# Kernel tuning notes

Hardware: AMD Instinct MI355X
Metric: run time of the kernel (lower is better)

Reference implementation:

```python
import jax, jax.numpy as jnp
import numpy as np

NUM_BINS = 23
SIGMA_RATIO = 0.5
SMOOTH_NR = 1e-07
SMOOTH_DR = 1e-07

BIN_CENTERS = jnp.linspace(0.0, 1.0, NUM_BINS)  # [bins]
_sigma = jnp.mean(BIN_CENTERS[1:] - BIN_CENTERS[:-1]) * SIGMA_RATIO
PRETERM = 1.0 / (2.0 * _sigma ** 2)


def setup_inputs() -> dict:
    key = jax.random.key(0)
    k1, k2 = jax.random.split(key)
    shape = (4, 1, 96, 96, 96)
    pred = jax.random.uniform(k1, shape, dtype=jnp.float32)
    target = jax.random.uniform(k2, shape, dtype=jnp.float32)
    return {"pred": pred, "target": target}


def _parzen(img):
    # img: [B, ...] -> weight [B, N, bins], probability [B, 1, bins]
    img = jnp.clip(img, 0.0, 1.0)
    img = img.reshape(img.shape[0], -1, 1)  # [B, N, 1]
    weight = jnp.exp(-PRETERM * (img - BIN_CENTERS[None, None, :]) ** 2)  # [B, N, bins]
    weight = weight / jnp.sum(weight, axis=-1, keepdims=True)
    probability = jnp.mean(weight, axis=-2, keepdims=True)  # [B, 1, bins]
    return weight, probability


def reference(pred, target):
    wa, pa = _parzen(pred)    # wa: [B, N, bins]
    wb, pb = _parzen(target)
    n = wa.shape[1]
    # joint histogram: [B, bins, bins]
    pab = jnp.einsum('bni,bnj->bij', wa, wb) / n
    # marginal product: [B, bins, bins]
    papb = jnp.einsum('bki,bkj->bij', pa, pb)
    mi = jnp.sum(pab * jnp.log((pab + SMOOTH_NR) / (papb + SMOOTH_DR) + SMOOTH_DR), axis=(1, 2))
    return -jnp.mean(mi)
```

## Files before the change

### kernel.cpp

```cpp
#include <hip/hip_runtime.h>
#include <math.h>


#define NBINS   23
#define NCELLS  529
#define NBATCH  4
#define NVOX    884736
#define PBLK    432
#define RPB     16
#define RBLK    (PBLK / RPB)
#define RS      72
#define IMGB    (32 * RS * 2)
#define WREG    (2 * IMGB)

typedef float    vf4  __attribute__((ext_vector_type(4)));
typedef _Float16 h8   __attribute__((ext_vector_type(8)));
typedef float    f16v __attribute__((ext_vector_type(16)));

#define G1 0.13533528f
#define G2 3.3546263e-4f
#define G3 1.5229979e-8f

__device__ __forceinline__ float window7(float x, int& i0, float* w)
{
    x = fminf(fmaxf(x, 0.0f), 1.0f);
    int ka = (int)floorf(fmaf(x, 22.0f, 0.5f));
    i0 = min(max(ka - 3, 0), 16);
    float v  = fmaf((float)(i0 + 3), -(1.0f / 22.0f), x);
    float W0 = __expf(-968.0f * v * v);
    float R  = __expf(88.0f * v);
    float Ri = __builtin_amdgcn_rcpf(R);
    float R2 = R * R,   R3 = R2 * R;
    float R2i = Ri * Ri, R3i = R2i * Ri;
    w[0] = W0 * (R3i * G3);
    w[1] = W0 * (R2i * G2);
    w[2] = W0 * (Ri  * G1);
    w[3] = W0;
    w[4] = W0 * (R   * G1);
    w[5] = W0 * (R2  * G2);
    w[6] = W0 * (R3  * G3);
    return ((w[0] + w[6]) + (w[1] + w[5])) + ((w[2] + w[4]) + w[3]);
}

__global__ __launch_bounds__(256)
void mi_mfma(const float* __restrict__ pred,
             const float* __restrict__ targ,
             float* __restrict__ partial)
{
    __shared__ __align__(16) char smem[4 * WREG];

    const int p    = blockIdx.x;
    const int b    = blockIdx.y;
    const int wv   = threadIdx.x >> 6;
    const int lane = threadIdx.x & 63;
    const int m    = lane & 31;
    const int h    = lane >> 5;

    char* wbase = smem + wv * WREG;
    _Float16* Aimg = (_Float16*)wbase;
    _Float16* Bimg = (_Float16*)(wbase + IMGB);

    const size_t base = (size_t)b * NVOX + (size_t)p * 2048 + (size_t)wv * 512
                      + (size_t)lane * 8;
    const vf4* __restrict__ px4 = (const vf4*)(pred + base);
    const vf4* __restrict__ py4 = (const vf4*)(targ + base);
    vf4 xa = px4[0], xb = px4[1], ya = py4[0], yb = py4[1];
    float xs[8] = {xa.x, xa.y, xa.z, xa.w, xb.x, xb.y, xb.z, xb.w};
    float ys[8] = {ya.x, ya.y, ya.z, ya.w, yb.x, yb.y, yb.z, yb.w};

    f16v acc = {};

    #pragma unroll
    for (int c = 0; c < 8; ++c) {
        vf4 z = {0.f, 0.f, 0.f, 0.f};
        #pragma unroll
        for (int it = 0; it < 3; ++it) {
            *(vf4*)(wbase        + (it * 64 + lane) * 16) = z;
            *(vf4*)(wbase + IMGB + (it * 64 + lane) * 16) = z;
        }
        if (lane < 24) {
            *(vf4*)(wbase        + (192 + lane) * 16) = z;
            *(vf4*)(wbase + IMGB + (192 + lane) * 16) = z;
        }

        int ia, ja;
        float wa[7], wb[7];
        float sa = window7(xs[c], ia, wa);
        float sb = window7(ys[c], ja, wb);
        float inv = __builtin_amdgcn_rcpf(sa * sb);

        #pragma unroll
        for (int t = 0; t < 7; ++t) {
            Aimg[(ia + t) * RS + lane] = (_Float16)(wa[t] * inv);
            Bimg[(ja + t) * RS + lane] = (_Float16)wb[t];
        }

        #pragma unroll
        for (int s = 0; s < 4; ++s) {
            h8 Af = *(const h8*)(Aimg + m * RS + 16 * s + 8 * h);
            h8 Bf = *(const h8*)(Bimg + m * RS + 16 * s + 8 * h);
            acc = __builtin_amdgcn_mfma_f32_32x32x16_f16(Af, Bf, acc, 0, 0, 0);
        }
    }

    float* tile = (float*)wbase;
    #pragma unroll
    for (int r = 0; r < 16; ++r) {
        int row = (r & 3) + 8 * (r >> 2) + 4 * h;
        tile[row * 33 + m] = acc[r];
    }
    __syncthreads();
    for (int c = threadIdx.x; c < NCELLS; c += 256) {
        int i = c / NBINS, j = c % NBINS;
        float s = 0.0f;
        #pragma unroll
        for (int w = 0; w < 4; ++w)
            s += ((const float*)(smem + w * WREG))[i * 33 + j];
        partial[((size_t)(b * PBLK + p)) * NCELLS + c] = s;
    }
}

__global__ __launch_bounds__(256)
void mi_reduce(const float* __restrict__ partial, double* __restrict__ pab64)
{
    const int g = blockIdx.x;
    const int b = blockIdx.y;
    const int t = threadIdx.x;
    const float* __restrict__ src =
        partial + ((size_t)b * PBLK + (size_t)g * RPB) * NCELLS;

    double a0 = 0.0, a1 = 0.0, a2 = 0.0;
    #pragma unroll
    for (int p = 0; p < RPB; ++p) {
        const float* __restrict__ row = src + (size_t)p * NCELLS;
        a0 += (double)row[t];
        a1 += (double)row[256 + t];
        if (t < NCELLS - 512) a2 += (double)row[512 + t];
    }
    atomicAdd(&pab64[b * NCELLS + t],       a0);
    atomicAdd(&pab64[b * NCELLS + 256 + t], a1);
    if (t < NCELLS - 512) atomicAdd(&pab64[b * NCELLS + 512 + t], a2);
}

__global__ __launch_bounds__(256)
void mi_final(const double* __restrict__ pab64, float* __restrict__ out)
{
    __shared__ double s_pab[NCELLS];
    __shared__ double s_pa[NBINS];
    __shared__ double s_pb[NBINS];
    __shared__ double s_red[4];

    double total = 0.0;
    for (int b = 0; b < NBATCH; ++b) {
        for (int c = threadIdx.x; c < NCELLS; c += 256)
            s_pab[c] = pab64[b * NCELLS + c] * (1.0 / (double)NVOX);
        __syncthreads();
        if (threadIdx.x < NBINS) {
            const int i = threadIdx.x;
            double r = 0.0, cl = 0.0;
            for (int j = 0; j < NBINS; ++j) {
                r  += s_pab[i * NBINS + j];
                cl += s_pab[j * NBINS + i];
            }
            s_pa[i] = r; s_pb[i] = cl;
        }
        __syncthreads();
        double t = 0.0;
        for (int c = threadIdx.x; c < NCELLS; c += 256) {
            double pv   = s_pab[c];
            double papb = s_pa[c / NBINS] * s_pb[c % NBINS];
            t += pv * log((pv + 1e-7) / (papb + 1e-7) + 1e-7);
        }
        #pragma unroll
        for (int off = 32; off > 0; off >>= 1) t += __shfl_down(t, off, 64);
        if ((threadIdx.x & 63) == 0) s_red[threadIdx.x >> 6] = t;
        __syncthreads();
        if (threadIdx.x == 0) total += s_red[0] + s_red[1] + s_red[2] + s_red[3];
        __syncthreads();
    }
    if (threadIdx.x == 0) out[0] = (float)(-total * 0.25);
}

extern "C" void kernel_launch(void* const* d_in, const int* in_sizes, int n_in,
                              void* d_out, int out_size, void* d_ws, size_t ws_size,
                              hipStream_t stream)
{
    const float* pred = (const float*)d_in[0];
    const float* targ = (const float*)d_in[1];
    float* out = (float*)d_out;
    char* ws = (char*)d_ws;

    const size_t off_partial = 0;
    const size_t off_pab64   =
        ((size_t)NBATCH * PBLK * NCELLS * 4 + 255) & ~(size_t)255;

    float*  partial = (float*)(ws + off_partial);
    double* pab64   = (double*)(ws + off_pab64);

    (void)hipMemsetAsync(pab64, 0, (size_t)NBATCH * NCELLS * sizeof(double), stream);
    mi_mfma  <<<dim3(PBLK, NBATCH), 256, 0, stream>>>(pred, targ, partial);
    mi_reduce<<<dim3(RBLK, NBATCH), 256, 0, stream>>>(partial, pab64);
    mi_final <<<1, 256, 0, stream>>>(pab64, out);
}
```

Baseline: 107.8 us.

## Fold memset and final kernel into neighbors, swizzle LDS weight images

Removes the hipMemsetAsync and the separate single-block final kernel. The first block of each batch in the MFMA kernel now zeroes the accumulators and the flag. The reduce kernel uses a last-block-done atomic counter to run the MI computation. It also XOR-swizzles the fp16 weight image columns in LDS to cut bank conflicts on the writes and MFMA operand reads. This trades launch overhead for threadfence and atomic-counter synchronization.

```diff
diff --git a/kernel.cpp b/kernel.cpp
--- a/kernel.cpp
+++ b/kernel.cpp
@@ -12,6 +12,8 @@
 #define RS      72
 #define IMGB    (32 * RS * 2)
 #define WREG    (2 * IMGB)
+
+#define SWZ(r, c) ((c) ^ (((r) & 7) << 3))
 
 typedef float    vf4  __attribute__((ext_vector_type(4)));
 typedef _Float16 h8   __attribute__((ext_vector_type(8)));
@@ -45,7 +47,9 @@
 __global__ __launch_bounds__(256)
 void mi_mfma(const float* __restrict__ pred,
              const float* __restrict__ targ,
-             float* __restrict__ partial)
+             float* __restrict__ partial,
+             double* __restrict__ pab64,
+             unsigned int* __restrict__ flag)
 {
     __shared__ __align__(16) char smem[4 * WREG];
 
@@ -55,6 +59,12 @@
     const int lane = threadIdx.x & 63;
     const int m    = lane & 31;
     const int h    = lane >> 5;
+
+    if (p == 0) {
+        for (int c = threadIdx.x; c < NCELLS; c += 256)
+            pab64[b * NCELLS + c] = 0.0;
+        if (b == 0 && threadIdx.x == 0) *flag = 0u;
+    }
 
     char* wbase = smem + wv * WREG;
     _Float16* Aimg = (_Float16*)wbase;
@@ -91,14 +101,15 @@
 
         #pragma unroll
         for (int t = 0; t < 7; ++t) {
-            Aimg[(ia + t) * RS + lane] = (_Float16)(wa[t] * inv);
-            Bimg[(ja + t) * RS + lane] = (_Float16)wb[t];
+            int ra = ia + t, rb = ja + t;
+            Aimg[ra * RS + SWZ(ra, lane)] = (_Float16)(wa[t] * inv);
+            Bimg[rb * RS + SWZ(rb, lane)] = (_Float16)wb[t];
         }
 
         #pragma unroll
         for (int s = 0; s < 4; ++s) {
-            h8 Af = *(const h8*)(Aimg + m * RS + 16 * s + 8 * h);
-            h8 Bf = *(const h8*)(Bimg + m * RS + 16 * s + 8 * h);
+            h8 Af = *(const h8*)(Aimg + m * RS + SWZ(m, 16 * s + 8 * h));
+            h8 Bf = *(const h8*)(Bimg + m * RS + SWZ(m, 16 * s + 8 * h));
             acc = __builtin_amdgcn_mfma_f32_32x32x16_f16(Af, Bf, acc, 0, 0, 0);
         }
     }
@@ -121,7 +132,10 @@
 }
 
 __global__ __launch_bounds__(256)
-void mi_reduce(const float* __restrict__ partial, double* __restrict__ pab64)
+void mi_reduce_final(const float* __restrict__ partial,
+                     double* __restrict__ pab64,
+                     unsigned int* __restrict__ flag,
+                     float* __restrict__ out)
 {
     const int g = blockIdx.x;
     const int b = blockIdx.y;
@@ -140,45 +154,52 @@
     atomicAdd(&pab64[b * NCELLS + t],       a0);
     atomicAdd(&pab64[b * NCELLS + 256 + t], a1);
     if (t < NCELLS - 512) atomicAdd(&pab64[b * NCELLS + 512 + t], a2);
-}
-
-__global__ __launch_bounds__(256)
-void mi_final(const double* __restrict__ pab64, float* __restrict__ out)
-{
+
+    __threadfence();
+    __shared__ int is_last;
+    if (t == 0)
+        is_last = (atomicAdd(flag, 1u) == (unsigned)(RBLK * NBATCH - 1));
+    __syncthreads();
+    if (!is_last) return;
+    __threadfence();
+
     __shared__ double s_pab[NCELLS];
     __shared__ double s_pa[NBINS];
     __shared__ double s_pb[NBINS];
     __shared__ double s_red[4];
 
     double total = 0.0;
-    for (int b = 0; b < NBATCH; ++b) {
-        for (int c = threadIdx.x; c < NCELLS; c += 256)
-            s_pab[c] = pab64[b * NCELLS + c] * (1.0 / (double)NVOX);
-        __syncthreads();
-        if (threadIdx.x < NBINS) {
-            const int i = threadIdx.x;
+    for (int bb = 0; bb < NBATCH; ++bb) {
+        for (int c = t; c < NCELLS; c += 256) {
+            double v = __hip_atomic_load(&pab64[bb * NCELLS + c],
+                                         __ATOMIC_RELAXED,
+                                         __HIP_MEMORY_SCOPE_AGENT);
+            s_pab[c] = v * (1.0 / (double)NVOX);
+        }
+        __syncthreads();
+        if (t < NBINS) {
             double r = 0.0, cl = 0.0;
             for (int j = 0; j < NBINS; ++j) {
-                r  += s_pab[i * NBINS + j];
-                cl += s_pab[j * NBINS + i];
+                r  += s_pab[t * NBINS + j];
+                cl += s_pab[j * NBINS + t];
             }
-            s_pa[i] = r; s_pb[i] = cl;
-        }
-        __syncthreads();
-        double t = 0.0;
-        for (int c = threadIdx.x; c < NCELLS; c += 256) {
+            s_pa[t] = r; s_pb[t] = cl;
+        }
+        __syncthreads();
+        double s = 0.0;
+        for (int c = t; c < NCELLS; c += 256) {
             double pv   = s_pab[c];
             double papb = s_pa[c / NBINS] * s_pb[c % NBINS];
-            t += pv * log((pv + 1e-7) / (papb + 1e-7) + 1e-7);
-        }
-        #pragma unroll
-        for (int off = 32; off > 0; off >>= 1) t += __shfl_down(t, off, 64);
-        if ((threadIdx.x & 63) == 0) s_red[threadIdx.x >> 6] = t;
-        __syncthreads();
-        if (threadIdx.x == 0) total += s_red[0] + s_red[1] + s_red[2] + s_red[3];
-        __syncthreads();
-    }
-    if (threadIdx.x == 0) out[0] = (float)(-total * 0.25);
+            s += pv * log((pv + 1e-7) / (papb + 1e-7) + 1e-7);
+        }
+        #pragma unroll
+        for (int off = 32; off > 0; off >>= 1) s += __shfl_down(s, off, 64);
+        if ((t & 63) == 0) s_red[t >> 6] = s;
+        __syncthreads();
+        if (t == 0) total += s_red[0] + s_red[1] + s_red[2] + s_red[3];
+        __syncthreads();
+    }
+    if (t == 0) out[0] = (float)(-total * 0.25);
 }
 
 extern "C" void kernel_launch(void* const* d_in, const int* in_sizes, int n_in,
@@ -193,12 +214,14 @@
     const size_t off_partial = 0;
     const size_t off_pab64   =
         ((size_t)NBATCH * PBLK * NCELLS * 4 + 255) & ~(size_t)255;
-
-    float*  partial = (float*)(ws + off_partial);
-    double* pab64   = (double*)(ws + off_pab64);
-
-    (void)hipMemsetAsync(pab64, 0, (size_t)NBATCH * NCELLS * sizeof(double), stream);
-    mi_mfma  <<<dim3(PBLK, NBATCH), 256, 0, stream>>>(pred, targ, partial);
-    mi_reduce<<<dim3(RBLK, NBATCH), 256, 0, stream>>>(partial, pab64);
-    mi_final <<<1, 256, 0, stream>>>(pab64, out);
-}
+    const size_t off_flag    = off_pab64 + (size_t)NBATCH * NCELLS * 8;
+
+    float*        partial = (float*)(ws + off_partial);
+    double*       pab64   = (double*)(ws + off_pab64);
+    unsigned int* flag    = (unsigned int*)(ws + off_flag);
+
+    mi_mfma<<<dim3(PBLK, NBATCH), 256, 0, stream>>>(pred, targ, partial,
+                                                    pab64, flag);
+    mi_reduce_final<<<dim3(RBLK, NBATCH), 256, 0, stream>>>(partial, pab64,
+                                                            flag, out);
+}
```

Measured after the change: 121.4 us. 12.5% more time.

## Shrink LDS images to 23 rows and give each wave nine voxel chunks

Applied to the files above, without the earlier changes.

Each LDS weight image now holds only 23 rows instead of 32. MFMA operand reads clamp rows 23 to 31 onto row 22, which cuts shared memory per block and the zeroing work per chunk. Launch bounds now ask for six blocks per CU. Each block covers 2304 voxels, so there are 384 blocks, and each wave loops over nine 64-voxel chunks using per-chunk nontemporal scalar loads instead of preloaded vec4 loads. The goal is higher occupancy and fewer blocks and partials to reduce, at the cost of a rolled loop with global load latency inside each iteration.

```diff
diff --git a/kernel.cpp b/kernel.cpp
--- a/kernel.cpp
+++ b/kernel.cpp
@@ -6,11 +6,14 @@
 #define NCELLS  529
 #define NBATCH  4
 #define NVOX    884736
-#define PBLK    432
+#define PBLK    384
+#define VPB     2304
+#define VPW     576
+#define NCHUNK  9
 #define RPB     16
 #define RBLK    (PBLK / RPB)
 #define RS      72
-#define IMGB    (32 * RS * 2)
+#define IMGB    (23 * RS * 2)
 #define WREG    (2 * IMGB)
 
 typedef float    vf4  __attribute__((ext_vector_type(4)));
@@ -42,7 +45,7 @@
     return ((w[0] + w[6]) + (w[1] + w[5])) + ((w[2] + w[4]) + w[3]);
 }
 
-__global__ __launch_bounds__(256)
+__global__ __launch_bounds__(256, 6)
 void mi_mfma(const float* __restrict__ pred,
              const float* __restrict__ targ,
              float* __restrict__ partial)
@@ -55,38 +58,36 @@
     const int lane = threadIdx.x & 63;
     const int m    = lane & 31;
     const int h    = lane >> 5;
+    const int mr   = m < NBINS ? m : NBINS - 1;
 
     char* wbase = smem + wv * WREG;
     _Float16* Aimg = (_Float16*)wbase;
     _Float16* Bimg = (_Float16*)(wbase + IMGB);
-
-    const size_t base = (size_t)b * NVOX + (size_t)p * 2048 + (size_t)wv * 512
-                      + (size_t)lane * 8;
-    const vf4* __restrict__ px4 = (const vf4*)(pred + base);
-    const vf4* __restrict__ py4 = (const vf4*)(targ + base);
-    vf4 xa = px4[0], xb = px4[1], ya = py4[0], yb = py4[1];
-    float xs[8] = {xa.x, xa.y, xa.z, xa.w, xb.x, xb.y, xb.z, xb.w};
-    float ys[8] = {ya.x, ya.y, ya.z, ya.w, yb.x, yb.y, yb.z, yb.w};
+    const _Float16* Ard = Aimg + mr * RS + 8 * h;
+    const _Float16* Brd = Bimg + mr * RS + 8 * h;
+
+    const float* __restrict__ px =
+        pred + (size_t)b * NVOX + (size_t)p * VPB + (size_t)wv * VPW;
+    const float* __restrict__ py =
+        targ + (size_t)b * NVOX + (size_t)p * VPB + (size_t)wv * VPW;
 
     f16v acc = {};
 
-    #pragma unroll
-    for (int c = 0; c < 8; ++c) {
+    for (int c = 0; c < NCHUNK; ++c) {
         vf4 z = {0.f, 0.f, 0.f, 0.f};
         #pragma unroll
-        for (int it = 0; it < 3; ++it) {
-            *(vf4*)(wbase        + (it * 64 + lane) * 16) = z;
-            *(vf4*)(wbase + IMGB + (it * 64 + lane) * 16) = z;
-        }
-        if (lane < 24) {
-            *(vf4*)(wbase        + (192 + lane) * 16) = z;
-            *(vf4*)(wbase + IMGB + (192 + lane) * 16) = z;
-        }
+        for (int it = 0; it < 6; ++it)
+            *(vf4*)(wbase + (it * 64 + lane) * 16) = z;
+        if (lane < 30)
+            *(vf4*)(wbase + (384 + lane) * 16) = z;
+
+        float x = __builtin_nontemporal_load(px + c * 64 + lane);
+        float y = __builtin_nontemporal_load(py + c * 64 + lane);
 
         int ia, ja;
         float wa[7], wb[7];
-        float sa = window7(xs[c], ia, wa);
-        float sb = window7(ys[c], ja, wb);
+        float sa = window7(x, ia, wa);
+        float sb = window7(y, ja, wb);
         float inv = __builtin_amdgcn_rcpf(sa * sb);
 
         #pragma unroll
@@ -97,8 +98,8 @@
 
         #pragma unroll
         for (int s = 0; s < 4; ++s) {
-            h8 Af = *(const h8*)(Aimg + m * RS + 16 * s + 8 * h);
-            h8 Bf = *(const h8*)(Bimg + m * RS + 16 * s + 8 * h);
+            h8 Af = *(const h8*)(Ard + 16 * s);
+            h8 Bf = *(const h8*)(Brd + 16 * s);
             acc = __builtin_amdgcn_mfma_f32_32x32x16_f16(Af, Bf, acc, 0, 0, 0);
         }
     }
```

After: 111.7 us. 3.6% more time.
